# Performance work log

Hardware: AMD Instinct MI355X
Metric: run time of the kernel (lower is better)

Reference implementation:

```python
import jax, jax.numpy as jnp
import numpy as np

N, E, FE = 20000, 160000, 500000
IN, HC, HEADS = 128, 64, 4
HEADC = HC // HEADS          # 16
DV = HEADC                   # 16
KHOP = 3
NUM_T = 128
OUT = 1
CST = 1e-5


def _lin(key, fan_in, fan_out):
    kw, kb = jax.random.split(key)
    s = 1.0 / np.sqrt(fan_in)
    W = jax.random.uniform(kw, (fan_in, fan_out), minval=-s, maxval=s, dtype=jnp.float32)
    b = jax.random.uniform(kb, (fan_out,), minval=-s, maxval=s, dtype=jnp.float32)
    return W, b


def setup_inputs() -> dict:
    key = jax.random.key(0)
    ks = jax.random.split(key, 16)
    x = jax.random.normal(ks[0], (N, IN), dtype=jnp.float32)
    edge_index = jax.random.randint(ks[1], (2, E), 0, N, dtype=jnp.int32)
    full_edge_index = jax.random.randint(ks[2], (2, FE), 0, N, dtype=jnp.int32)
    time_steps = jax.random.randint(ks[3], (N,), 0, NUM_T, dtype=jnp.int32)
    Wi, bi = _lin(ks[4], IN, HC)
    Wt1, bt1 = _lin(ks[5], HC, 4 * HC)
    Wt2, bt2 = _lin(ks[6], 4 * HC, HC)
    WQ, bQ = _lin(ks[7], HC, HEADS * HEADC)
    WK, bK = _lin(ks[8], HC, HEADS * HEADC)
    WV, bV = _lin(ks[9], HC, HEADS * DV)
    Wo, bo = _lin(ks[10], HEADS * DV, DV)
    hopwise = jnp.ones((KHOP + 1,), dtype=jnp.float32)
    headwise = jnp.zeros((HEADS, KHOP), dtype=jnp.float32)
    Wf1, bf1 = _lin(ks[11], 2 * DV, DV)
    Wf2, bf2 = _lin(ks[12], DV, OUT)
    return dict(x=x, edge_index=edge_index, full_edge_index=full_edge_index,
                time_steps=time_steps, Wi=Wi, bi=bi, Wt1=Wt1, bt1=bt1,
                Wt2=Wt2, bt2=bt2, WQ=WQ, bQ=bQ, WK=WK, bK=bK, WV=WV, bV=bV,
                Wo=Wo, bo=bo, hopwise=hopwise, headwise=headwise,
                Wf1=Wf1, bf1=bf1, Wf2=Wf2, bf2=bf2)


def _sin_emb(t, dim, num_steps, rescale=4000.0):
    # Sinusoidal timestep embedding rescaled by num_steps (diffusion style).
    t = t.astype(jnp.float32) * (rescale / num_steps)
    half = dim // 2
    freqs = jnp.exp(-jnp.log(10000.0) / (half - 1) * jnp.arange(half, dtype=jnp.float32))
    args = t[:, None] * freqs[None, :]
    return jnp.concatenate([jnp.sin(args), jnp.cos(args)], axis=-1)


def reference(x, edge_index, full_edge_index, time_steps,
              Wi, bi, Wt1, bt1, Wt2, bt2, WQ, bQ, WK, bK, WV, bV,
              Wo, bo, hopwise, headwise, Wf1, bf1, Wf2, bf2):
    n = x.shape[0]
    row, col = edge_index[0], edge_index[1]

    # random-walk norm: deg over destination (col), norm gathered at source (row)
    deg = jax.ops.segment_sum(jnp.ones_like(col, dtype=x.dtype), col, num_segments=n)
    deg_inv = jnp.where(deg > 0, 1.0 / deg, 0.0)
    norm = deg_inv[row]                                   # [E]

    t_emb = _sin_emb(time_steps, HC, NUM_T)               # [N, HC]
    t_emb = jax.nn.silu(t_emb @ Wt1 + bt1) @ Wt2 + bt2    # [N, HC]

    h = jax.nn.relu(x @ Wi + bi + t_emb)                  # [N, HC]

    Q = (1.0 + jax.nn.elu(h @ WQ + bQ)).reshape(n, HEADS, HEADC)
    Kf = (1.0 + jax.nn.elu(h @ WK + bK)).reshape(n, HEADS, HEADC)
    V = (h @ WV + bV).reshape(n, HEADS, DV)

    M = jnp.einsum('nhi,nhj->nhij', Kf, V)                # [N, H, hc, dv]
    hidden = V * hopwise[0]
    layerwise = jax.nn.softmax(headwise, axis=0)          # softmax over heads

    for hop in range(KHOP):
        # gather-scale-scatter message passing (random walk propagation)
        M = jax.ops.segment_sum(M[row] * norm[:, None, None, None], col, num_segments=n)
        Kf = jax.ops.segment_sum(Kf[row] * norm[:, None, None], col, num_segments=n)
        H = jnp.einsum('nhi,nhij->nhj', Q, M)             # [N, H, dv]
        C = jnp.einsum('nhi,nhi->nh', Q, Kf)[..., None] + CST
        gamma = hopwise[hop + 1] * layerwise[:, hop][:, None]   # [H, 1]
        hidden = hidden + gamma * (H / C)

    # multi_concat output projection
    hidden = hidden.reshape(n, HEADS * DV) @ Wo + bo      # [N, DV]

    src, dst = full_edge_index[0], full_edge_index[1]
    he = jnp.concatenate([hidden[src], hidden[dst]], axis=-1)  # [FE, 2*DV]
    edge_logits = jax.nn.silu(he @ Wf1 + bf1) @ Wf2 + bf2      # [FE, OUT]
    return edge_logits, hidden
```

## Files before the change

### kernel.cpp

```cpp
#include <hip/hip_runtime.h>
#include <hip/hip_bf16.h>
#include <math.h>


#define HC 64
#define HEADS 4
#define HEADC 16
#define DV 16
#define KHOP 3
#define NUM_T 128
#define MSZ 1024
#define CST 1e-5f

typedef float f32x2 __attribute__((ext_vector_type(2)));

__device__ __forceinline__ float bf_lo(unsigned int u) { return __uint_as_float(u << 16); }
__device__ __forceinline__ float bf_hi(unsigned int u) { return __uint_as_float(u & 0xffff0000u); }
__device__ __forceinline__ float bf2f(unsigned short s) { return __uint_as_float(((unsigned int)s) << 16); }
__device__ __forceinline__ unsigned short f2bf(float f) {
    unsigned int u = __float_as_uint(f);
    u = (u + 0x7fffu + ((u >> 16) & 1u)) >> 16;
    return (unsigned short)u;
}
__device__ __forceinline__ unsigned int pack4fp8(float a, float b, float c, float d) {
    int r = __builtin_amdgcn_cvt_pk_fp8_f32(a, b, 0, false);
    r = __builtin_amdgcn_cvt_pk_fp8_f32(c, d, r, true);
    return (unsigned int)r;
}

__global__ void k_deg(const int* __restrict__ col, int* __restrict__ deg, int E) {
    int e = blockIdx.x * 256 + threadIdx.x;
    if (e < E) atomicAdd(&deg[col[e]], 1);
}

__global__ void k_scan_a(const int* __restrict__ deg, int* __restrict__ row_ptr,
                         int* __restrict__ blk_sums, int n) {
    __shared__ int buf[256];
    int i = blockIdx.x * 256 + threadIdx.x;
    int v = (i < n) ? deg[i] : 0;
    buf[threadIdx.x] = v;
    __syncthreads();
    for (int off = 1; off < 256; off <<= 1) {
        int t = (threadIdx.x >= off) ? buf[threadIdx.x - off] : 0;
        __syncthreads();
        buf[threadIdx.x] += t;
        __syncthreads();
    }
    if (i < n) row_ptr[i] = buf[threadIdx.x] - v;
    if (threadIdx.x == 255) blk_sums[blockIdx.x] = buf[255];
}

__global__ void k_scan_b(int* __restrict__ blk_sums, int nb, int* __restrict__ row_ptr, int n) {
    __shared__ int buf[256];
    int t = threadIdx.x;
    int v = (t < nb) ? blk_sums[t] : 0;
    buf[t] = v;
    __syncthreads();
    for (int off = 1; off < 256; off <<= 1) {
        int u = (t >= off) ? buf[t - off] : 0;
        __syncthreads();
        buf[t] += u;
        __syncthreads();
    }
    if (t < nb) blk_sums[t] = buf[t] - v;
    if (t == 255) row_ptr[n] = buf[255];
}

__global__ void k_scan_c(const int* __restrict__ deg, const int* __restrict__ blk_sums,
                         int* __restrict__ row_ptr, int* __restrict__ fill_off,
                         float* __restrict__ deg_inv, int n) {
    int i = blockIdx.x * 256 + threadIdx.x;
    if (i >= n) return;
    int e = row_ptr[i] + blk_sums[blockIdx.x];
    row_ptr[i] = e;
    fill_off[i] = e;
    int d = deg[i];
    deg_inv[i] = (d > 0) ? 1.0f / (float)d : 0.0f;
}

__global__ void k_fill(const int* __restrict__ row, const int* __restrict__ col,
                       const float* __restrict__ deg_inv, int* __restrict__ fill_off,
                       int* __restrict__ src_sorted, float* __restrict__ w_sorted, int E) {
    int e = blockIdx.x * 256 + threadIdx.x;
    if (e >= E) return;
    int c = col[e];
    int r = row[e];
    int pos = atomicAdd(&fill_off[c], 1);
    src_sorted[pos] = r;
    w_sorted[pos] = deg_inv[r];
}

__global__ __launch_bounds__(256) void k_temb(
    const float* __restrict__ Wt1, const float* __restrict__ bt1,
    const float* __restrict__ Wt2, const float* __restrict__ bt2,
    const float* __restrict__ hopwise, const float* __restrict__ headwise,
    float* __restrict__ gamma, float* __restrict__ table) {
    if (blockIdx.x == 0 && threadIdx.x == 0) {
        for (int k = 0; k < KHOP; k++) {
            float m = -1e30f;
            for (int h2 = 0; h2 < HEADS; h2++) m = fmaxf(m, headwise[h2 * KHOP + k]);
            float ex[HEADS]; float s = 0.f;
            for (int h2 = 0; h2 < HEADS; h2++) { ex[h2] = expf(headwise[h2 * KHOP + k] - m); s += ex[h2]; }
            for (int h2 = 0; h2 < HEADS; h2++) gamma[k * HEADS + h2] = hopwise[k + 1] * ex[h2] / s;
        }
    }
    int slot = threadIdx.x >> 6;
    int j = threadIdx.x & 63;
    int tval = blockIdx.x * 4 + slot;
    __shared__ float emb_s[4][64];
    __shared__ float z1_s[4][256];
    {
        float t = (float)tval * 31.25f;
        float e;
        if (j < 32) e = sinf(t * expf(-0.2971077539347156f * (float)j));
        else        e = cosf(t * expf(-0.2971077539347156f * (float)(j - 32)));
        emb_s[slot][j] = e;
    }
    __syncthreads();
    {
        #pragma unroll
        for (int k = 0; k < 4; k++) {
            int o = j + 64 * k;
            float acc = bt1[o];
            for (int i = 0; i < 64; i++) acc += emb_s[slot][i] * Wt1[i * 256 + o];
            z1_s[slot][o] = acc / (1.f + expf(-acc));
        }
    }
    __syncthreads();
    {
        float acc = bt2[j];
        for (int i = 0; i < 256; i++) acc += z1_s[slot][i] * Wt2[i * 64 + j];
        table[tval * 64 + j] = acc;
    }
}

__global__ __launch_bounds__(256) void k_node(
    const float* __restrict__ x, const int* __restrict__ time_steps,
    const float* __restrict__ temb, const float* __restrict__ Wi,
    const float* __restrict__ bi,
    const float* __restrict__ WQ, const float* __restrict__ bQ,
    const float* __restrict__ WK, const float* __restrict__ bK,
    const float* __restrict__ WV, const float* __restrict__ bV,
    const float* __restrict__ hopwise,
    float* __restrict__ Q, unsigned short* __restrict__ Kf0,
    unsigned short* __restrict__ V0, float* __restrict__ hidden, int n) {
    __shared__ float xs[32][128];
    __shared__ float hs[32][64];
    int j = threadIdx.x & 63;
    int slot = threadIdx.x >> 6;
    int nbase = blockIdx.x * 32;
    int nvalid = min(32, n - nbase);
    const float4* xg = (const float4*)(x + (size_t)nbase * 128);
    float4* xs4 = (float4*)&xs[0][0];
    for (int idx = threadIdx.x; idx < nvalid * 32; idx += 256) xs4[idx] = xg[idx];
    __syncthreads();
    int nl = slot * 8;
    {
        float acc[8];
        #pragma unroll
        for (int k = 0; k < 8; k++) acc[k] = 0.f;
        #pragma unroll 4
        for (int i = 0; i < 128; i++) {
            float w = Wi[i * 64 + j];
            #pragma unroll
            for (int k = 0; k < 8; k++) acc[k] += xs[nl + k][i] * w;
        }
        float bj = bi[j];
        #pragma unroll
        for (int k = 0; k < 8; k++) {
            int node = nbase + nl + k;
            float te = (node < n) ? temb[time_steps[node] * 64 + j] : 0.f;
            hs[nl + k][j] = fmaxf(acc[k] + bj + te, 0.f);
        }
    }
    __syncthreads();
    float aq[8], ak[8], av[8];
    #pragma unroll
    for (int k = 0; k < 8; k++) { aq[k] = bQ[j]; ak[k] = bK[j]; av[k] = bV[j]; }
    #pragma unroll 2
    for (int i = 0; i < 64; i++) {
        float wq = WQ[i * 64 + j], wk = WK[i * 64 + j], wv = WV[i * 64 + j];
        #pragma unroll
        for (int k = 0; k < 8; k++) {
            float hv = hs[nl + k][i];
            aq[k] += hv * wq; ak[k] += hv * wk; av[k] += hv * wv;
        }
    }
    float h0 = hopwise[0];
    #pragma unroll
    for (int k = 0; k < 8; k++) {
        int node = nbase + nl + k;
        if (node < n) {
            float q  = 1.f + ((aq[k] > 0.f) ? aq[k] : (expf(aq[k]) - 1.f));
            float kf = 1.f + ((ak[k] > 0.f) ? ak[k] : (expf(ak[k]) - 1.f));
            Q[(size_t)node * 64 + j] = q;
            Kf0[(size_t)node * 64 + j] = f2bf(kf);
            V0[(size_t)node * 64 + j] = f2bf(av[k]);
            hidden[(size_t)node * 64 + j] = av[k] * h0;
        }
    }
}

__global__ __launch_bounds__(256) void k_hop1(
    const unsigned short* __restrict__ Kf0, const unsigned short* __restrict__ V0,
    const int* __restrict__ row_ptr, const int* __restrict__ src_sorted,
    const float* __restrict__ w_sorted, const float* __restrict__ Q,
    const float* __restrict__ gamma,
    unsigned char* __restrict__ M1, unsigned short* __restrict__ Kf1,
    float* __restrict__ hidden) {
    int node = blockIdx.x;
    int tid = threadIdx.x;
    int h = tid >> 6, i = (tid >> 2) & 15, jb = (tid & 3) * 4;
    __shared__ float sm[MSZ];
    __shared__ float sk[64];
    float4 acc = make_float4(0.f, 0.f, 0.f, 0.f);
    float kacc = 0.f;
    int beg = row_ptr[node], end = row_ptr[node + 1];
    int e = beg;
    for (; e + 4 <= end; e += 4) {
        int s0 = src_sorted[e + 0], s1 = src_sorted[e + 1];
        int s2 = src_sorted[e + 2], s3 = src_sorted[e + 3];
        float w0 = w_sorted[e + 0], w1 = w_sorted[e + 1];
        float w2 = w_sorted[e + 2], w3 = w_sorted[e + 3];
        float kf0v = bf2f(Kf0[(size_t)s0 * 64 + h * 16 + i]);
        float kf1v = bf2f(Kf0[(size_t)s1 * 64 + h * 16 + i]);
        float kf2v = bf2f(Kf0[(size_t)s2 * 64 + h * 16 + i]);
        float kf3v = bf2f(Kf0[(size_t)s3 * 64 + h * 16 + i]);
        uint2 v0 = *(const uint2*)(V0 + (size_t)s0 * 64 + h * 16 + jb);
        uint2 v1 = *(const uint2*)(V0 + (size_t)s1 * 64 + h * 16 + jb);
        uint2 v2 = *(const uint2*)(V0 + (size_t)s2 * 64 + h * 16 + jb);
        uint2 v3 = *(const uint2*)(V0 + (size_t)s3 * 64 + h * 16 + jb);
        float kr0 = 0.f, kr1 = 0.f, kr2 = 0.f, kr3 = 0.f;
        if (tid < 64) {
            kr0 = bf2f(Kf0[(size_t)s0 * 64 + tid]);
            kr1 = bf2f(Kf0[(size_t)s1 * 64 + tid]);
            kr2 = bf2f(Kf0[(size_t)s2 * 64 + tid]);
            kr3 = bf2f(Kf0[(size_t)s3 * 64 + tid]);
        }
        float a0 = w0 * kf0v, a1 = w1 * kf1v, a2 = w2 * kf2v, a3 = w3 * kf3v;
        acc.x += a0 * bf_lo(v0.x) + a1 * bf_lo(v1.x) + a2 * bf_lo(v2.x) + a3 * bf_lo(v3.x);
        acc.y += a0 * bf_hi(v0.x) + a1 * bf_hi(v1.x) + a2 * bf_hi(v2.x) + a3 * bf_hi(v3.x);
        acc.z += a0 * bf_lo(v0.y) + a1 * bf_lo(v1.y) + a2 * bf_lo(v2.y) + a3 * bf_lo(v3.y);
        acc.w += a0 * bf_hi(v0.y) + a1 * bf_hi(v1.y) + a2 * bf_hi(v2.y) + a3 * bf_hi(v3.y);
        if (tid < 64) kacc += w0 * kr0 + w1 * kr1 + w2 * kr2 + w3 * kr3;
    }
    for (; e < end; e++) {
        int s = src_sorted[e];
        float ww = w_sorted[e];
        float kf = bf2f(Kf0[(size_t)s * 64 + h * 16 + i]);
        uint2 vv = *(const uint2*)(V0 + (size_t)s * 64 + h * 16 + jb);
        float wk = ww * kf;
        acc.x += wk * bf_lo(vv.x); acc.y += wk * bf_hi(vv.x);
        acc.z += wk * bf_lo(vv.y); acc.w += wk * bf_hi(vv.y);
        if (tid < 64) kacc += ww * bf2f(Kf0[(size_t)s * 64 + tid]);
    }
    *(unsigned int*)(M1 + (size_t)node * MSZ + tid * 4) = pack4fp8(acc.x, acc.y, acc.z, acc.w);
    if (tid < 64) Kf1[(size_t)node * 64 + tid] = f2bf(kacc);
    ((float4*)sm)[tid] = acc;
    if (tid < 64) sk[tid] = kacc;
    __syncthreads();
    if (tid < 64) {
        int hh = tid >> 4, j = tid & 15;
        const float* qn = Q + (size_t)node * 64 + hh * 16;
        float C = CST, H = 0.f;
        #pragma unroll
        for (int ii = 0; ii < 16; ii++) {
            float qv = qn[ii];
            C += qv * sk[hh * 16 + ii];
            H += qv * sm[hh * 256 + ii * 16 + j];
        }
        float g = gamma[0 * HEADS + hh];
        hidden[(size_t)node * 64 + tid] += g * H / C;
    }
}

__global__ __launch_bounds__(256) void k_hop23(
    const unsigned char* __restrict__ Mold, const unsigned short* __restrict__ Kfold,
    const int* __restrict__ row_ptr, const int* __restrict__ src_sorted,
    const float* __restrict__ w_sorted, const float* __restrict__ Q,
    const float* __restrict__ gamma,
    unsigned char* __restrict__ Mnew, unsigned short* __restrict__ Kfnew,
    float* __restrict__ hidden, int hop, int write_out,
    const float* __restrict__ Wo, const float* __restrict__ bo,
    float* __restrict__ out16) {
    int node = blockIdx.x;
    int tid = threadIdx.x;
    __shared__ float sm[MSZ];
    __shared__ float sk[64];
    __shared__ float sh[64];
    float4 acc = make_float4(0.f, 0.f, 0.f, 0.f);
    float kacc = 0.f;
    int beg = row_ptr[node], end = row_ptr[node + 1];
    int e = beg;
    for (; e + 4 <= end; e += 4) {
        int s0 = src_sorted[e + 0], s1 = src_sorted[e + 1];
        int s2 = src_sorted[e + 2], s3 = src_sorted[e + 3];
        float w0 = w_sorted[e + 0], w1 = w_sorted[e + 1];
        float w2 = w_sorted[e + 2], w3 = w_sorted[e + 3];
        unsigned int m0 = *(const unsigned int*)(Mold + (size_t)s0 * MSZ + tid * 4);
        unsigned int m1 = *(const unsigned int*)(Mold + (size_t)s1 * MSZ + tid * 4);
        unsigned int m2 = *(const unsigned int*)(Mold + (size_t)s2 * MSZ + tid * 4);
        unsigned int m3 = *(const unsigned int*)(Mold + (size_t)s3 * MSZ + tid * 4);
        float kr0 = 0.f, kr1 = 0.f, kr2 = 0.f, kr3 = 0.f;
        if (tid < 64) {
            kr0 = bf2f(Kfold[(size_t)s0 * 64 + tid]);
            kr1 = bf2f(Kfold[(size_t)s1 * 64 + tid]);
            kr2 = bf2f(Kfold[(size_t)s2 * 64 + tid]);
            kr3 = bf2f(Kfold[(size_t)s3 * 64 + tid]);
        }
        f32x2 d0l = __builtin_amdgcn_cvt_pk_f32_fp8((int)m0, false);
        f32x2 d0h = __builtin_amdgcn_cvt_pk_f32_fp8((int)m0, true);
        f32x2 d1l = __builtin_amdgcn_cvt_pk_f32_fp8((int)m1, false);
        f32x2 d1h = __builtin_amdgcn_cvt_pk_f32_fp8((int)m1, true);
        f32x2 d2l = __builtin_amdgcn_cvt_pk_f32_fp8((int)m2, false);
        f32x2 d2h = __builtin_amdgcn_cvt_pk_f32_fp8((int)m2, true);
        f32x2 d3l = __builtin_amdgcn_cvt_pk_f32_fp8((int)m3, false);
        f32x2 d3h = __builtin_amdgcn_cvt_pk_f32_fp8((int)m3, true);
        acc.x += w0 * d0l.x + w1 * d1l.x + w2 * d2l.x + w3 * d3l.x;
        acc.y += w0 * d0l.y + w1 * d1l.y + w2 * d2l.y + w3 * d3l.y;
        acc.z += w0 * d0h.x + w1 * d1h.x + w2 * d2h.x + w3 * d3h.x;
        acc.w += w0 * d0h.y + w1 * d1h.y + w2 * d2h.y + w3 * d3h.y;
        if (tid < 64) kacc += w0 * kr0 + w1 * kr1 + w2 * kr2 + w3 * kr3;
    }
    for (; e < end; e++) {
        int s = src_sorted[e];
        float ww = w_sorted[e];
        unsigned int mv = *(const unsigned int*)(Mold + (size_t)s * MSZ + tid * 4);
        f32x2 dl = __builtin_amdgcn_cvt_pk_f32_fp8((int)mv, false);
        f32x2 dh = __builtin_amdgcn_cvt_pk_f32_fp8((int)mv, true);
        acc.x += ww * dl.x; acc.y += ww * dl.y;
        acc.z += ww * dh.x; acc.w += ww * dh.y;
        if (tid < 64) kacc += ww * bf2f(Kfold[(size_t)s * 64 + tid]);
    }
    if (write_out) {
        *(unsigned int*)(Mnew + (size_t)node * MSZ + tid * 4) = pack4fp8(acc.x, acc.y, acc.z, acc.w);
        if (tid < 64) Kfnew[(size_t)node * 64 + tid] = f2bf(kacc);
    }
    ((float4*)sm)[tid] = acc;
    if (tid < 64) sk[tid] = kacc;
    __syncthreads();
    if (tid < 64) {
        int hh = tid >> 4, j = tid & 15;
        const float* qn = Q + (size_t)node * 64 + hh * 16;
        float C = CST, H = 0.f;
        #pragma unroll
        for (int i = 0; i < 16; i++) {
            float qv = qn[i];
            C += qv * sk[hh * 16 + i];
            H += qv * sm[hh * 256 + i * 16 + j];
        }
        float g = gamma[hop * HEADS + hh];
        float hid = hidden[(size_t)node * 64 + tid] + g * H / C;
        if (write_out) hidden[(size_t)node * 64 + tid] = hid;
        else sh[tid] = hid;
    }
    if (!write_out) {
        __syncthreads();
        if (tid < 16) {
            float a = bo[tid];
            #pragma unroll 8
            for (int i = 0; i < 64; i++) a += sh[i] * Wo[i * 16 + tid];
            out16[(size_t)node * 16 + tid] = a;
        }
    }
}

__global__ __launch_bounds__(256) void k_edge(
    const int* __restrict__ src, const int* __restrict__ dst,
    const float* __restrict__ hid16,
    const float* __restrict__ Wf1, const float* __restrict__ bf1,
    const float* __restrict__ Wf2, const float* __restrict__ bf2,
    float* __restrict__ out, int fe) {
    __shared__ float w1[512];
    __shared__ float b1[16];
    __shared__ float w2[16];
    __shared__ float b2s;
    int t = threadIdx.x;
    for (int i = t; i < 512; i += 256) w1[i] = Wf1[i];
    if (t < 16) { b1[t] = bf1[t]; w2[t] = Wf2[t]; }
    if (t == 0) b2s = bf2[0];
    __syncthreads();
    int e = blockIdx.x * 256 + t;
    if (e >= fe) return;
    int s = src[e], d = dst[e];
    float he[32];
    const float4* hs4 = (const float4*)(hid16 + (size_t)s * 16);
    const float4* hd4 = (const float4*)(hid16 + (size_t)d * 16);
    #pragma unroll
    for (int q = 0; q < 4; q++) {
        float4 v = hs4[q];
        he[q * 4 + 0] = v.x; he[q * 4 + 1] = v.y; he[q * 4 + 2] = v.z; he[q * 4 + 3] = v.w;
        float4 w = hd4[q];
        he[16 + q * 4 + 0] = w.x; he[16 + q * 4 + 1] = w.y; he[16 + q * 4 + 2] = w.z; he[16 + q * 4 + 3] = w.w;
    }
    float acc = b2s;
    #pragma unroll
    for (int o = 0; o < 16; o++) {
        float z = b1[o];
        #pragma unroll
        for (int i = 0; i < 32; i++) z += he[i] * w1[i * 16 + o];
        z = z / (1.f + expf(-z));
        acc += z * w2[o];
    }
    out[e] = acc;
}

extern "C" void kernel_launch(void* const* d_in, const int* in_sizes, int n_in,
                              void* d_out, int out_size, void* d_ws, size_t ws_size,
                              hipStream_t stream) {
    const float* x        = (const float*)d_in[0];
    const int*   eidx     = (const int*)d_in[1];
    const int*   feidx    = (const int*)d_in[2];
    const int*   tsteps   = (const int*)d_in[3];
    const float* Wi  = (const float*)d_in[4];
    const float* bi  = (const float*)d_in[5];
    const float* Wt1 = (const float*)d_in[6];
    const float* bt1 = (const float*)d_in[7];
    const float* Wt2 = (const float*)d_in[8];
    const float* bt2 = (const float*)d_in[9];
    const float* WQ  = (const float*)d_in[10];
    const float* bQ  = (const float*)d_in[11];
    const float* WK  = (const float*)d_in[12];
    const float* bK  = (const float*)d_in[13];
    const float* WV  = (const float*)d_in[14];
    const float* bV  = (const float*)d_in[15];
    const float* Wo  = (const float*)d_in[16];
    const float* bo  = (const float*)d_in[17];
    const float* hopwise  = (const float*)d_in[18];
    const float* headwise = (const float*)d_in[19];
    const float* Wf1 = (const float*)d_in[20];
    const float* bf1 = (const float*)d_in[21];
    const float* Wf2 = (const float*)d_in[22];
    const float* bf2 = (const float*)d_in[23];

    const int N  = in_sizes[3];
    const int E  = in_sizes[1] / 2;
    const int FE = in_sizes[2] / 2;
    const int* row = eidx;
    const int* col = eidx + E;
    const int* fsrc = feidx;
    const int* fdst = feidx + FE;
    const int nb = (N + 255) / 256;

    char* ws = (char*)d_ws;
    size_t off = 0;
    auto alloc = [&](size_t bytes) -> char* {
        char* p = ws + off;
        off = (off + bytes + 255) & ~(size_t)255;
        return p;
    };
    float* gamma     = (float*)alloc(KHOP * HEADS * sizeof(float));
    int*   deg_cnt   = (int*)alloc((size_t)N * 4);
    float* deg_inv   = (float*)alloc((size_t)N * 4);
    int*   row_ptr   = (int*)alloc((size_t)(N + 1) * 4);
    int*   fill_off  = (int*)alloc((size_t)N * 4);
    int*   blk_sums  = (int*)alloc((size_t)nb * 4);
    int*   src_sorted= (int*)alloc((size_t)E * 4);
    float* w_sorted  = (float*)alloc((size_t)E * 4);
    float* temb      = (float*)alloc((size_t)NUM_T * HC * 4);
    float* Qbuf      = (float*)alloc((size_t)N * HC * 4);
    unsigned short* Kf0 = (unsigned short*)alloc((size_t)N * HC * 2);
    unsigned short* V0  = (unsigned short*)alloc((size_t)N * HC * 2);
    unsigned short* Kf_a = (unsigned short*)alloc((size_t)N * HC * 2);
    unsigned short* Kf_b = (unsigned short*)alloc((size_t)N * HC * 2);
    float* hidden    = (float*)alloc((size_t)N * HC * 4);
    unsigned char* M_a = (unsigned char*)alloc((size_t)N * MSZ);
    unsigned char* M_b = (unsigned char*)alloc((size_t)N * MSZ);
    (void)ws_size;

    float* out_edges = (float*)d_out;
    float* out_hid16 = (float*)d_out + FE;

    (void)hipMemsetAsync(deg_cnt, 0, (size_t)N * 4, stream);
    k_deg<<<(E + 255) / 256, 256, 0, stream>>>(col, deg_cnt, E);
    k_scan_a<<<nb, 256, 0, stream>>>(deg_cnt, row_ptr, blk_sums, N);
    k_scan_b<<<1, 256, 0, stream>>>(blk_sums, nb, row_ptr, N);
    k_scan_c<<<nb, 256, 0, stream>>>(deg_cnt, blk_sums, row_ptr, fill_off, deg_inv, N);
    k_fill<<<(E + 255) / 256, 256, 0, stream>>>(row, col, deg_inv, fill_off, src_sorted, w_sorted, E);
    k_temb<<<NUM_T / 4, 256, 0, stream>>>(Wt1, bt1, Wt2, bt2, hopwise, headwise, gamma, temb);
    k_node<<<(N + 31) / 32, 256, 0, stream>>>(x, tsteps, temb, Wi, bi,
                                              WQ, bQ, WK, bK, WV, bV, hopwise,
                                              Qbuf, Kf0, V0, hidden, N);
    k_hop1<<<N, 256, 0, stream>>>(Kf0, V0, row_ptr, src_sorted, w_sorted, Qbuf, gamma,
                                  M_a, Kf_a, hidden);
    k_hop23<<<N, 256, 0, stream>>>(M_a, Kf_a, row_ptr, src_sorted, w_sorted, Qbuf, gamma,
                                   M_b, Kf_b, hidden, 1, 1, Wo, bo, out_hid16);
    k_hop23<<<N, 256, 0, stream>>>(M_b, Kf_b, row_ptr, src_sorted, w_sorted, Qbuf, gamma,
                                   M_a, Kf_a, hidden, 2, 0, Wo, bo, out_hid16);
    k_edge<<<(FE + 255) / 256, 256, 0, stream>>>(fsrc, fdst, out_hid16, Wf1, bf1, Wf2, bf2,
                                                 out_edges, FE);
}
```

Measured before the change: 305.5 us.

## Precompute fp8 M0 in node kernel and map one wave per node in hops

The node kernel now builds the initial outer-product state K⊗V as fp8 directly in a new M_0 buffer. This drops the special first-hop kernel, and all three hops use one generic gather kernel. That kernel assigns a single 64-lane wave per destination node, four nodes per block, with each lane loading 16 fp8 bytes per neighbour. The aim is fewer idle threads and wider, better-coalesced loads. In exchange, hop 1 now reads 1 KB per neighbour instead of bf16 K and V, and the node kernel writes an extra 20 MB state buffer. Rounding V⊗K to fp8 before the first aggregation also adds some precision loss.

```diff
diff --git a/kernel.cpp b/kernel.cpp
--- a/kernel.cpp
+++ b/kernel.cpp
@@ -14,8 +14,6 @@
 
 typedef float f32x2 __attribute__((ext_vector_type(2)));
 
-__device__ __forceinline__ float bf_lo(unsigned int u) { return __uint_as_float(u << 16); }
-__device__ __forceinline__ float bf_hi(unsigned int u) { return __uint_as_float(u & 0xffff0000u); }
 __device__ __forceinline__ float bf2f(unsigned short s) { return __uint_as_float(((unsigned int)s) << 16); }
 __device__ __forceinline__ unsigned short f2bf(float f) {
     unsigned int u = __float_as_uint(f);
@@ -143,9 +141,11 @@
     const float* __restrict__ WV, const float* __restrict__ bV,
     const float* __restrict__ hopwise,
     float* __restrict__ Q, unsigned short* __restrict__ Kf0,
-    unsigned short* __restrict__ V0, float* __restrict__ hidden, int n) {
+    unsigned char* __restrict__ M0, float* __restrict__ hidden, int n) {
     __shared__ float xs[32][128];
     __shared__ float hs[32][64];
+    __shared__ unsigned short ksh[32][64];
+    __shared__ unsigned short vsh[32][64];
     int j = threadIdx.x & 63;
     int slot = threadIdx.x >> 6;
     int nbase = blockIdx.x * 32;
@@ -190,91 +190,32 @@
     #pragma unroll
     for (int k = 0; k < 8; k++) {
         int node = nbase + nl + k;
+        float q  = 1.f + ((aq[k] > 0.f) ? aq[k] : (expf(aq[k]) - 1.f));
+        float kf = 1.f + ((ak[k] > 0.f) ? ak[k] : (expf(ak[k]) - 1.f));
+        unsigned short kb = f2bf(kf), vb = f2bf(av[k]);
+        ksh[nl + k][j] = kb;
+        vsh[nl + k][j] = vb;
         if (node < n) {
-            float q  = 1.f + ((aq[k] > 0.f) ? aq[k] : (expf(aq[k]) - 1.f));
-            float kf = 1.f + ((ak[k] > 0.f) ? ak[k] : (expf(ak[k]) - 1.f));
             Q[(size_t)node * 64 + j] = q;
-            Kf0[(size_t)node * 64 + j] = f2bf(kf);
-            V0[(size_t)node * 64 + j] = f2bf(av[k]);
+            Kf0[(size_t)node * 64 + j] = kb;
             hidden[(size_t)node * 64 + j] = av[k] * h0;
         }
     }
-}
-
-__global__ __launch_bounds__(256) void k_hop1(
-    const unsigned short* __restrict__ Kf0, const unsigned short* __restrict__ V0,
-    const int* __restrict__ row_ptr, const int* __restrict__ src_sorted,
-    const float* __restrict__ w_sorted, const float* __restrict__ Q,
-    const float* __restrict__ gamma,
-    unsigned char* __restrict__ M1, unsigned short* __restrict__ Kf1,
-    float* __restrict__ hidden) {
-    int node = blockIdx.x;
-    int tid = threadIdx.x;
-    int h = tid >> 6, i = (tid >> 2) & 15, jb = (tid & 3) * 4;
-    __shared__ float sm[MSZ];
-    __shared__ float sk[64];
-    float4 acc = make_float4(0.f, 0.f, 0.f, 0.f);
-    float kacc = 0.f;
-    int beg = row_ptr[node], end = row_ptr[node + 1];
-    int e = beg;
-    for (; e + 4 <= end; e += 4) {
-        int s0 = src_sorted[e + 0], s1 = src_sorted[e + 1];
-        int s2 = src_sorted[e + 2], s3 = src_sorted[e + 3];
-        float w0 = w_sorted[e + 0], w1 = w_sorted[e + 1];
-        float w2 = w_sorted[e + 2], w3 = w_sorted[e + 3];
-        float kf0v = bf2f(Kf0[(size_t)s0 * 64 + h * 16 + i]);
-        float kf1v = bf2f(Kf0[(size_t)s1 * 64 + h * 16 + i]);
-        float kf2v = bf2f(Kf0[(size_t)s2 * 64 + h * 16 + i]);
-        float kf3v = bf2f(Kf0[(size_t)s3 * 64 + h * 16 + i]);
-        uint2 v0 = *(const uint2*)(V0 + (size_t)s0 * 64 + h * 16 + jb);
-        uint2 v1 = *(const uint2*)(V0 + (size_t)s1 * 64 + h * 16 + jb);
-        uint2 v2 = *(const uint2*)(V0 + (size_t)s2 * 64 + h * 16 + jb);
-        uint2 v3 = *(const uint2*)(V0 + (size_t)s3 * 64 + h * 16 + jb);
-        float kr0 = 0.f, kr1 = 0.f, kr2 = 0.f, kr3 = 0.f;
-        if (tid < 64) {
-            kr0 = bf2f(Kf0[(size_t)s0 * 64 + tid]);
-            kr1 = bf2f(Kf0[(size_t)s1 * 64 + tid]);
-            kr2 = bf2f(Kf0[(size_t)s2 * 64 + tid]);
-            kr3 = bf2f(Kf0[(size_t)s3 * 64 + tid]);
-        }
-        float a0 = w0 * kf0v, a1 = w1 * kf1v, a2 = w2 * kf2v, a3 = w3 * kf3v;
-        acc.x += a0 * bf_lo(v0.x) + a1 * bf_lo(v1.x) + a2 * bf_lo(v2.x) + a3 * bf_lo(v3.x);
-        acc.y += a0 * bf_hi(v0.x) + a1 * bf_hi(v1.x) + a2 * bf_hi(v2.x) + a3 * bf_hi(v3.x);
-        acc.z += a0 * bf_lo(v0.y) + a1 * bf_lo(v1.y) + a2 * bf_lo(v2.y) + a3 * bf_lo(v3.y);
-        acc.w += a0 * bf_hi(v0.y) + a1 * bf_hi(v1.y) + a2 * bf_hi(v2.y) + a3 * bf_hi(v3.y);
-        if (tid < 64) kacc += w0 * kr0 + w1 * kr1 + w2 * kr2 + w3 * kr3;
-    }
-    for (; e < end; e++) {
-        int s = src_sorted[e];
-        float ww = w_sorted[e];
-        float kf = bf2f(Kf0[(size_t)s * 64 + h * 16 + i]);
-        uint2 vv = *(const uint2*)(V0 + (size_t)s * 64 + h * 16 + jb);
-        float wk = ww * kf;
-        acc.x += wk * bf_lo(vv.x); acc.y += wk * bf_hi(vv.x);
-        acc.z += wk * bf_lo(vv.y); acc.w += wk * bf_hi(vv.y);
-        if (tid < 64) kacc += ww * bf2f(Kf0[(size_t)s * 64 + tid]);
-    }
-    *(unsigned int*)(M1 + (size_t)node * MSZ + tid * 4) = pack4fp8(acc.x, acc.y, acc.z, acc.w);
-    if (tid < 64) Kf1[(size_t)node * 64 + tid] = f2bf(kacc);
-    ((float4*)sm)[tid] = acc;
-    if (tid < 64) sk[tid] = kacc;
-    __syncthreads();
-    if (tid < 64) {
-        int hh = tid >> 4, j = tid & 15;
-        const float* qn = Q + (size_t)node * 64 + hh * 16;
-        float C = CST, H = 0.f;
-        #pragma unroll
-        for (int ii = 0; ii < 16; ii++) {
-            float qv = qn[ii];
-            C += qv * sk[hh * 16 + ii];
-            H += qv * sm[hh * 256 + ii * 16 + j];
-        }
-        float g = gamma[0 * HEADS + hh];
-        hidden[(size_t)node * 64 + tid] += g * H / C;
-    }
-}
-
-__global__ __launch_bounds__(256) void k_hop23(
+    __syncthreads();
+    int t = threadIdx.x;
+    int h2 = t >> 6, i2 = (t >> 2) & 15, jb = (t & 3) * 4;
+    for (int k = 0; k < nvalid; k++) {
+        float kf = bf2f(ksh[k][h2 * 16 + i2]);
+        float v0 = bf2f(vsh[k][h2 * 16 + jb + 0]);
+        float v1 = bf2f(vsh[k][h2 * 16 + jb + 1]);
+        float v2 = bf2f(vsh[k][h2 * 16 + jb + 2]);
+        float v3 = bf2f(vsh[k][h2 * 16 + jb + 3]);
+        *(unsigned int*)(M0 + (size_t)(nbase + k) * MSZ + t * 4) =
+            pack4fp8(kf * v0, kf * v1, kf * v2, kf * v3);
+    }
+}
+
+__global__ __launch_bounds__(256) void k_hop(
     const unsigned char* __restrict__ Mold, const unsigned short* __restrict__ Kfold,
     const int* __restrict__ row_ptr, const int* __restrict__ src_sorted,
     const float* __restrict__ w_sorted, const float* __restrict__ Q,
@@ -282,85 +223,105 @@
     unsigned char* __restrict__ Mnew, unsigned short* __restrict__ Kfnew,
     float* __restrict__ hidden, int hop, int write_out,
     const float* __restrict__ Wo, const float* __restrict__ bo,
-    float* __restrict__ out16) {
-    int node = blockIdx.x;
-    int tid = threadIdx.x;
-    __shared__ float sm[MSZ];
-    __shared__ float sk[64];
-    __shared__ float sh[64];
-    float4 acc = make_float4(0.f, 0.f, 0.f, 0.f);
+    float* __restrict__ out16, int n) {
+    int wave = threadIdx.x >> 6;
+    int lane = threadIdx.x & 63;
+    int node = blockIdx.x * 4 + wave;
+    __shared__ float sm[4][MSZ];
+    __shared__ float sk[4][64];
+    __shared__ float sh[4][64];
+    bool valid = (node < n);
+    float acc[16];
+    #pragma unroll
+    for (int t = 0; t < 16; t++) acc[t] = 0.f;
     float kacc = 0.f;
-    int beg = row_ptr[node], end = row_ptr[node + 1];
-    int e = beg;
-    for (; e + 4 <= end; e += 4) {
-        int s0 = src_sorted[e + 0], s1 = src_sorted[e + 1];
-        int s2 = src_sorted[e + 2], s3 = src_sorted[e + 3];
-        float w0 = w_sorted[e + 0], w1 = w_sorted[e + 1];
-        float w2 = w_sorted[e + 2], w3 = w_sorted[e + 3];
-        unsigned int m0 = *(const unsigned int*)(Mold + (size_t)s0 * MSZ + tid * 4);
-        unsigned int m1 = *(const unsigned int*)(Mold + (size_t)s1 * MSZ + tid * 4);
-        unsigned int m2 = *(const unsigned int*)(Mold + (size_t)s2 * MSZ + tid * 4);
-        unsigned int m3 = *(const unsigned int*)(Mold + (size_t)s3 * MSZ + tid * 4);
-        float kr0 = 0.f, kr1 = 0.f, kr2 = 0.f, kr3 = 0.f;
-        if (tid < 64) {
-            kr0 = bf2f(Kfold[(size_t)s0 * 64 + tid]);
-            kr1 = bf2f(Kfold[(size_t)s1 * 64 + tid]);
-            kr2 = bf2f(Kfold[(size_t)s2 * 64 + tid]);
-            kr3 = bf2f(Kfold[(size_t)s3 * 64 + tid]);
-        }
-        f32x2 d0l = __builtin_amdgcn_cvt_pk_f32_fp8((int)m0, false);
-        f32x2 d0h = __builtin_amdgcn_cvt_pk_f32_fp8((int)m0, true);
-        f32x2 d1l = __builtin_amdgcn_cvt_pk_f32_fp8((int)m1, false);
-        f32x2 d1h = __builtin_amdgcn_cvt_pk_f32_fp8((int)m1, true);
-        f32x2 d2l = __builtin_amdgcn_cvt_pk_f32_fp8((int)m2, false);
-        f32x2 d2h = __builtin_amdgcn_cvt_pk_f32_fp8((int)m2, true);
-        f32x2 d3l = __builtin_amdgcn_cvt_pk_f32_fp8((int)m3, false);
-        f32x2 d3h = __builtin_amdgcn_cvt_pk_f32_fp8((int)m3, true);
-        acc.x += w0 * d0l.x + w1 * d1l.x + w2 * d2l.x + w3 * d3l.x;
-        acc.y += w0 * d0l.y + w1 * d1l.y + w2 * d2l.y + w3 * d3l.y;
-        acc.z += w0 * d0h.x + w1 * d1h.x + w2 * d2h.x + w3 * d3h.x;
-        acc.w += w0 * d0h.y + w1 * d1h.y + w2 * d2h.y + w3 * d3h.y;
-        if (tid < 64) kacc += w0 * kr0 + w1 * kr1 + w2 * kr2 + w3 * kr3;
-    }
-    for (; e < end; e++) {
-        int s = src_sorted[e];
-        float ww = w_sorted[e];
-        unsigned int mv = *(const unsigned int*)(Mold + (size_t)s * MSZ + tid * 4);
-        f32x2 dl = __builtin_amdgcn_cvt_pk_f32_fp8((int)mv, false);
-        f32x2 dh = __builtin_amdgcn_cvt_pk_f32_fp8((int)mv, true);
-        acc.x += ww * dl.x; acc.y += ww * dl.y;
-        acc.z += ww * dh.x; acc.w += ww * dh.y;
-        if (tid < 64) kacc += ww * bf2f(Kfold[(size_t)s * 64 + tid]);
-    }
-    if (write_out) {
-        *(unsigned int*)(Mnew + (size_t)node * MSZ + tid * 4) = pack4fp8(acc.x, acc.y, acc.z, acc.w);
-        if (tid < 64) Kfnew[(size_t)node * 64 + tid] = f2bf(kacc);
-    }
-    ((float4*)sm)[tid] = acc;
-    if (tid < 64) sk[tid] = kacc;
-    __syncthreads();
-    if (tid < 64) {
-        int hh = tid >> 4, j = tid & 15;
+    if (valid) {
+        int beg = row_ptr[node], end = row_ptr[node + 1];
+        int e = beg;
+        for (; e + 4 <= end; e += 4) {
+            int s0 = src_sorted[e + 0], s1 = src_sorted[e + 1];
+            int s2 = src_sorted[e + 2], s3 = src_sorted[e + 3];
+            float w0 = w_sorted[e + 0], w1 = w_sorted[e + 1];
+            float w2 = w_sorted[e + 2], w3 = w_sorted[e + 3];
+            uint4 m0 = *(const uint4*)(Mold + (size_t)s0 * MSZ + lane * 16);
+            uint4 m1 = *(const uint4*)(Mold + (size_t)s1 * MSZ + lane * 16);
+            uint4 m2 = *(const uint4*)(Mold + (size_t)s2 * MSZ + lane * 16);
+            uint4 m3 = *(const uint4*)(Mold + (size_t)s3 * MSZ + lane * 16);
+            unsigned short k0 = Kfold[(size_t)s0 * 64 + lane];
+            unsigned short k1 = Kfold[(size_t)s1 * 64 + lane];
+            unsigned short k2 = Kfold[(size_t)s2 * 64 + lane];
+            unsigned short k3 = Kfold[(size_t)s3 * 64 + lane];
+            const uint4 mm[4] = {m0, m1, m2, m3};
+            const float ww[4] = {w0, w1, w2, w3};
+            #pragma unroll
+            for (int u = 0; u < 4; u++) {
+                float wc = ww[u];
+                f32x2 p;
+                p = __builtin_amdgcn_cvt_pk_f32_fp8((int)mm[u].x, false); acc[0] += wc * p.x; acc[1] += wc * p.y;
+                p = __builtin_amdgcn_cvt_pk_f32_fp8((int)mm[u].x, true);  acc[2] += wc * p.x; acc[3] += wc * p.y;
+                p = __builtin_amdgcn_cvt_pk_f32_fp8((int)mm[u].y, false); acc[4] += wc * p.x; acc[5] += wc * p.y;
+                p = __builtin_amdgcn_cvt_pk_f32_fp8((int)mm[u].y, true);  acc[6] += wc * p.x; acc[7] += wc * p.y;
+                p = __builtin_amdgcn_cvt_pk_f32_fp8((int)mm[u].z, false); acc[8] += wc * p.x; acc[9] += wc * p.y;
+                p = __builtin_amdgcn_cvt_pk_f32_fp8((int)mm[u].z, true);  acc[10] += wc * p.x; acc[11] += wc * p.y;
+                p = __builtin_amdgcn_cvt_pk_f32_fp8((int)mm[u].w, false); acc[12] += wc * p.x; acc[13] += wc * p.y;
+                p = __builtin_amdgcn_cvt_pk_f32_fp8((int)mm[u].w, true);  acc[14] += wc * p.x; acc[15] += wc * p.y;
+            }
+            kacc += w0 * bf2f(k0) + w1 * bf2f(k1) + w2 * bf2f(k2) + w3 * bf2f(k3);
+        }
+        for (; e < end; e++) {
+            int s = src_sorted[e];
+            float wc = w_sorted[e];
+            uint4 mv = *(const uint4*)(Mold + (size_t)s * MSZ + lane * 16);
+            f32x2 p;
+            p = __builtin_amdgcn_cvt_pk_f32_fp8((int)mv.x, false); acc[0] += wc * p.x; acc[1] += wc * p.y;
+            p = __builtin_amdgcn_cvt_pk_f32_fp8((int)mv.x, true);  acc[2] += wc * p.x; acc[3] += wc * p.y;
+            p = __builtin_amdgcn_cvt_pk_f32_fp8((int)mv.y, false); acc[4] += wc * p.x; acc[5] += wc * p.y;
+            p = __builtin_amdgcn_cvt_pk_f32_fp8((int)mv.y, true);  acc[6] += wc * p.x; acc[7] += wc * p.y;
+            p = __builtin_amdgcn_cvt_pk_f32_fp8((int)mv.z, false); acc[8] += wc * p.x; acc[9] += wc * p.y;
+            p = __builtin_amdgcn_cvt_pk_f32_fp8((int)mv.z, true);  acc[10] += wc * p.x; acc[11] += wc * p.y;
+            p = __builtin_amdgcn_cvt_pk_f32_fp8((int)mv.w, false); acc[12] += wc * p.x; acc[13] += wc * p.y;
+            p = __builtin_amdgcn_cvt_pk_f32_fp8((int)mv.w, true);  acc[14] += wc * p.x; acc[15] += wc * p.y;
+            kacc += wc * bf2f(Kfold[(size_t)s * 64 + lane]);
+        }
+        if (write_out) {
+            uint4 st;
+            st.x = pack4fp8(acc[0], acc[1], acc[2], acc[3]);
+            st.y = pack4fp8(acc[4], acc[5], acc[6], acc[7]);
+            st.z = pack4fp8(acc[8], acc[9], acc[10], acc[11]);
+            st.w = pack4fp8(acc[12], acc[13], acc[14], acc[15]);
+            *(uint4*)(Mnew + (size_t)node * MSZ + lane * 16) = st;
+            Kfnew[(size_t)node * 64 + lane] = f2bf(kacc);
+        }
+        float4* smw = (float4*)&sm[wave][lane * 16];
+        smw[0] = make_float4(acc[0], acc[1], acc[2], acc[3]);
+        smw[1] = make_float4(acc[4], acc[5], acc[6], acc[7]);
+        smw[2] = make_float4(acc[8], acc[9], acc[10], acc[11]);
+        smw[3] = make_float4(acc[12], acc[13], acc[14], acc[15]);
+        sk[wave][lane] = kacc;
+    }
+    __syncthreads();
+    if (valid) {
+        int hh = lane >> 4, j = lane & 15;
         const float* qn = Q + (size_t)node * 64 + hh * 16;
         float C = CST, H = 0.f;
         #pragma unroll
         for (int i = 0; i < 16; i++) {
             float qv = qn[i];
-            C += qv * sk[hh * 16 + i];
-            H += qv * sm[hh * 256 + i * 16 + j];
+            C += qv * sk[wave][hh * 16 + i];
+            H += qv * sm[wave][hh * 256 + i * 16 + j];
         }
         float g = gamma[hop * HEADS + hh];
-        float hid = hidden[(size_t)node * 64 + tid] + g * H / C;
-        if (write_out) hidden[(size_t)node * 64 + tid] = hid;
-        else sh[tid] = hid;
+        float hid = hidden[(size_t)node * 64 + lane] + g * H / C;
+        if (write_out) hidden[(size_t)node * 64 + lane] = hid;
+        else sh[wave][lane] = hid;
     }
     if (!write_out) {
         __syncthreads();
-        if (tid < 16) {
-            float a = bo[tid];
+        if (valid && lane < 16) {
+            float a = bo[lane];
             #pragma unroll 8
-            for (int i = 0; i < 64; i++) a += sh[i] * Wo[i * 16 + tid];
-            out16[(size_t)node * 16 + tid] = a;
+            for (int i = 0; i < 64; i++) a += sh[wave][i] * Wo[i * 16 + lane];
+            out16[(size_t)node * 16 + lane] = a;
         }
     }
 }
@@ -459,11 +420,11 @@
     float* w_sorted  = (float*)alloc((size_t)E * 4);
     float* temb      = (float*)alloc((size_t)NUM_T * HC * 4);
     float* Qbuf      = (float*)alloc((size_t)N * HC * 4);
-    unsigned short* Kf0 = (unsigned short*)alloc((size_t)N * HC * 2);
-    unsigned short* V0  = (unsigned short*)alloc((size_t)N * HC * 2);
+    unsigned short* Kf0  = (unsigned short*)alloc((size_t)N * HC * 2);
     unsigned short* Kf_a = (unsigned short*)alloc((size_t)N * HC * 2);
     unsigned short* Kf_b = (unsigned short*)alloc((size_t)N * HC * 2);
     float* hidden    = (float*)alloc((size_t)N * HC * 4);
+    unsigned char* M_0 = (unsigned char*)alloc((size_t)N * MSZ);
     unsigned char* M_a = (unsigned char*)alloc((size_t)N * MSZ);
     unsigned char* M_b = (unsigned char*)alloc((size_t)N * MSZ);
     (void)ws_size;
@@ -480,13 +441,13 @@
     k_temb<<<NUM_T / 4, 256, 0, stream>>>(Wt1, bt1, Wt2, bt2, hopwise, headwise, gamma, temb);
     k_node<<<(N + 31) / 32, 256, 0, stream>>>(x, tsteps, temb, Wi, bi,
                                               WQ, bQ, WK, bK, WV, bV, hopwise,
-                                              Qbuf, Kf0, V0, hidden, N);
-    k_hop1<<<N, 256, 0, stream>>>(Kf0, V0, row_ptr, src_sorted, w_sorted, Qbuf, gamma,
-                                  M_a, Kf_a, hidden);
-    k_hop23<<<N, 256, 0, stream>>>(M_a, Kf_a, row_ptr, src_sorted, w_sorted, Qbuf, gamma,
-                                   M_b, Kf_b, hidden, 1, 1, Wo, bo, out_hid16);
-    k_hop23<<<N, 256, 0, stream>>>(M_b, Kf_b, row_ptr, src_sorted, w_sorted, Qbuf, gamma,
-                                   M_a, Kf_a, hidden, 2, 0, Wo, bo, out_hid16);
+                                              Qbuf, Kf0, M_0, hidden, N);
+    k_hop<<<(N + 3) / 4, 256, 0, stream>>>(M_0, Kf0, row_ptr, src_sorted, w_sorted, Qbuf, gamma,
+                                           M_a, Kf_a, hidden, 0, 1, Wo, bo, out_hid16, N);
+    k_hop<<<(N + 3) / 4, 256, 0, stream>>>(M_a, Kf_a, row_ptr, src_sorted, w_sorted, Qbuf, gamma,
+                                           M_b, Kf_b, hidden, 1, 1, Wo, bo, out_hid16, N);
+    k_hop<<<(N + 3) / 4, 256, 0, stream>>>(M_b, Kf_b, row_ptr, src_sorted, w_sorted, Qbuf, gamma,
+                                           M_a, Kf_a, hidden, 2, 0, Wo, bo, out_hid16, N);
     k_edge<<<(FE + 255) / 256, 256, 0, stream>>>(fsrc, fdst, out_hid16, Wf1, bf1, Wf2, bf2,
                                                  out_edges, FE);
 }
```

After: 307.4 us. About the same (+0.6%).
